# Optimization experiments

Hardware: AMD Instinct MI355X
Metric: run time of the kernel (lower is better)

## Reference

```python
import jax, jax.numpy as jnp
import numpy as np

DG = 4      # deformable groups
KS = 3      # kernel size
PAD = (KS - 1) // 2


def _deform_conv2d(x, offset, weight, dg=DG, pad=PAD):
    """Deformable conv v1 (stride 1, dilation 1, same padding, no bias).
    x:      [B, Cin, H, W]
    offset: [B, dg*2*K, H, W], layout (g, k, {y,x}) in channel dim
    weight: [Cout, Cin, kh, kw]
    """
    B, Cin, H, W = x.shape
    Cout, _, kh, kw = weight.shape
    K = kh * kw
    Cg = Cin // dg
    off = offset.reshape(B, dg, K, 2, H, W)
    # kernel tap coordinates, flattened row-major
    ky = jnp.repeat(jnp.arange(kh), kw).astype(x.dtype)   # [K]
    kx = jnp.tile(jnp.arange(kw), kh).astype(x.dtype)     # [K]
    # sampling positions [B, dg, K, H, W]
    py = off[:, :, :, 0] + (jnp.arange(H, dtype=x.dtype)[None, None, None, :, None]
                            + ky[None, None, :, None, None] - pad)
    px = off[:, :, :, 1] + (jnp.arange(W, dtype=x.dtype)[None, None, None, None, :]
                            + kx[None, None, :, None, None] - pad)
    y0 = jnp.floor(py)
    x0 = jnp.floor(px)
    xg = x.reshape(B, dg, Cg, H * W)
    val = jnp.zeros((B, dg, Cg, K, H, W), x.dtype)
    for dy in (0.0, 1.0):
        for dx in (0.0, 1.0):
            yc = y0 + dy
            xc = x0 + dx
            w = (1.0 - jnp.abs(py - yc)) * (1.0 - jnp.abs(px - xc))
            valid = (yc >= 0) & (yc <= H - 1) & (xc >= 0) & (xc <= W - 1)
            w = jnp.where(valid, w, 0.0)                      # zero padding
            idx = (jnp.clip(yc, 0, H - 1).astype(jnp.int32) * W
                   + jnp.clip(xc, 0, W - 1).astype(jnp.int32))  # [B,dg,K,H,W]
            idx_b = jnp.broadcast_to(idx.reshape(B, dg, 1, K * H * W),
                                     (B, dg, Cg, K * H * W))
            g = jnp.take_along_axis(xg, idx_b, axis=3).reshape(B, dg, Cg, K, H, W)
            val = val + w[:, :, None] * g
    # grouped-offset but dense conv: contract over (dg, Cg, K)
    wk = weight.reshape(Cout, dg, Cg, K)
    return jnp.einsum('bgckhw,ogck->bohw', val, wk)


def setup_inputs() -> dict:
    key = jax.random.key(0)
    k1, k2, k3, k4, k5, k6 = jax.random.split(key, 6)
    B, C, H, W = 2, 256, 64, 64
    reg_feat = jax.random.normal(k1, (B, C, H, W), jnp.float32)
    cls_feat = jax.random.normal(k2, (B, C, H, W), jnp.float32)
    pred_init = jax.random.normal(k3, (B, 34, H, W), jnp.float32)
    w_offset = jax.random.normal(k4, (DG * 2 * KS * KS, 34), jnp.float32) * 0.1
    w_reg = jax.random.normal(k5, (C, C, KS, KS), jnp.float32) * 0.01
    w_cls = jax.random.normal(k6, (C, C, KS, KS), jnp.float32) * 0.01
    return {"reg_feat": reg_feat, "cls_feat": cls_feat, "pred_init": pred_init,
            "w_offset": w_offset, "w_reg": w_reg, "w_cls": w_cls}


def reference(reg_feat, cls_feat, pred_init, w_offset, w_reg, w_cls):
    # 1x1 conv (bias-free) predicting offsets from detached anchor predictions
    offset = jnp.einsum('oc,bchw->bohw', w_offset, jax.lax.stop_gradient(pred_init))
    reg_refine = jax.nn.relu(_deform_conv2d(reg_feat, offset, w_reg))
    cls_refine = jax.nn.relu(_deform_conv2d(cls_feat, offset, w_cls))
    return (reg_refine, cls_refine)
```

## Files before the change

### kernel.cpp

```cpp
#include <hip/hip_runtime.h>
#include <hip/hip_bf16.h>
#include <stdint.h>

#define HW   4096
#define NB   2

typedef float f32x4 __attribute__((ext_vector_type(4)));
typedef short s16x8 __attribute__((ext_vector_type(8)));

__device__ __forceinline__ unsigned short f2bf(float f) {
    union { float f; unsigned int u; } v; v.f = f;
    unsigned int u = v.u;
    unsigned int r = (u + 0x7FFFu + ((u >> 16) & 1u)) >> 16;
    return (unsigned short)r;
}

__device__ __forceinline__ float bf2f(unsigned short u) {
    union { unsigned int u; float f; } v; v.u = ((unsigned int)u) << 16;
    return v.f;
}

__global__ void __launch_bounds__(256)
k_prep(const float* __restrict__ pred, const float* __restrict__ wo,
       const float* __restrict__ regf, const float* __restrict__ clsf,
       const float* __restrict__ wr,   const float* __restrict__ wc,
       float4* __restrict__ wbuf, int4* __restrict__ ibuf,
       unsigned short* __restrict__ fbuf, unsigned short* __restrict__ wfrag) {
    int bb = blockIdx.x;
    if (bb < 1152) {
        int loc = bb * 256 + threadIdx.x;
        int p  = loc & 4095;
        int g  = (loc >> 12) & 3;
        int bk = loc >> 14;
        int b  = bk / 9;
        int k  = bk - b * 9;
        int rowy = ((g * 9 + k) * 2) * 34;
        float oy = 0.f, ox = 0.f;
        const float* pb = pred + (size_t)b * 34 * HW + p;
        #pragma unroll
        for (int c = 0; c < 34; ++c) {
            float pv = pb[c * HW];
            oy += wo[rowy + c]      * pv;
            ox += wo[rowy + 34 + c] * pv;
        }
        int h = p >> 6, w = p & 63;
        int ky = k / 3, kx = k - ky * 3;
        float py = oy + (float)(h + ky - 1);
        float px = ox + (float)(w + kx - 1);
        float fy0 = floorf(py), fx0 = floorf(px);
        int y0 = (int)fy0, x0 = (int)fx0;
        float fy = py - fy0, fx = px - fx0;
        float wy0 = 1.f - fy, wy1 = fy, wx0 = 1.f - fx, wx1 = fx;
        if (!(y0 >= 0  && y0 <= 63)) wy0 = 0.f;
        if (!(y0 >= -1 && y0 <= 62)) wy1 = 0.f;
        if (!(x0 >= 0  && x0 <= 63)) wx0 = 0.f;
        if (!(x0 >= -1 && x0 <= 62)) wx1 = 0.f;
        int cy0 = min(max(y0, 0), 63),     cy1 = min(max(y0 + 1, 0), 63);
        int cx0 = min(max(x0, 0), 63),     cx1 = min(max(x0 + 1, 0), 63);
        wbuf[loc] = make_float4(wy0 * wx0, wy0 * wx1, wy1 * wx0, wy1 * wx1);
        ibuf[loc] = make_int4((cy0 * 64 + cx0) << 9, (cy0 * 64 + cx1) << 9,
                              (cy1 * 64 + cx0) << 9, (cy1 * 64 + cx1) << 9);
    } else if (bb < 2176) {
        __shared__ float tile[64][65];
        int bid = bb - 1152;
        int pt = bid & 63;
        int cb = (bid >> 6) & 3;
        int b  = (bid >> 8) & 1;
        int cv = bid >> 9;
        const float* src = cv ? clsf : regf;
        int t = threadIdx.x;
        int pl = t & 63, q = t >> 6;
        #pragma unroll
        for (int i = 0; i < 16; ++i) {
            int cl = q + i * 4;
            tile[cl][pl] = src[((size_t)(b * 256 + cb * 64 + cl)) * HW + pt * 64 + pl];
        }
        __syncthreads();
        int cpair = t & 31, prow = t >> 5;
        #pragma unroll
        for (int i = 0; i < 8; ++i) {
            int p = i * 8 + prow;
            unsigned int u0 = f2bf(tile[cpair * 2][p]);
            unsigned int u1 = f2bf(tile[cpair * 2 + 1][p]);
            *(unsigned int*)&fbuf[((size_t)((cv * 2 + b) * HW + pt * 64 + p)) * 256
                                  + cb * 64 + cpair * 2] = u0 | (u1 << 16);
        }
    } else {
        int L = (bb - 2176) * 256 + threadIdx.x;
        int conv = L / 73728;
        int r = L - conv * 73728;
        int lane = r & 63;
        int ot = (r >> 6) & 15;
        int kk = (r >> 10) & 1;
        int s  = r >> 11;
        int k = s >> 2, g = s & 3;
        int o  = ot * 16 + (lane & 15);
        int cb = kk * 32 + (lane >> 4) * 8;
        const float* w = conv ? wc : wr;
        s16x8 v;
        #pragma unroll
        for (int j = 0; j < 8; ++j) {
            int c = cb + j;
            v[j] = (short)f2bf(w[((size_t)o * 256 + g * 64 + c) * 9 + k]);
        }
        *(s16x8*)(wfrag + (size_t)L * 8) = v;
    }
}

__global__ void __launch_bounds__(512, 2)
k_main(const float4* __restrict__ wbuf, const int4* __restrict__ ibuf,
       const unsigned short* __restrict__ fbuf, const unsigned short* __restrict__ wfrag,
       float* __restrict__ out) {
    __shared__ __align__(16) unsigned short vt[2][64][72];

    int bid0 = blockIdx.x;
    int bid = (bid0 & 7) * 32 + (bid0 >> 3);
    int conv = bid >> 7;
    int b    = (bid >> 6) & 1;
    int pt   = bid & 63;
    int p0   = pt * 64;

    int tid  = threadIdx.x;
    int lane = tid & 63;
    int wo   = tid >> 6;
    int px   = tid >> 3;
    int cg   = tid & 7;

    const char* fbb = (const char*)(fbuf + (size_t)(conv * 2 + b) * HW * 256);
    const unsigned short* wfc = wfrag + (size_t)conv * 73728 * 8;

    f32x4 acc[2][4];
    #pragma unroll
    for (int i = 0; i < 2; ++i)
        #pragma unroll
        for (int j = 0; j < 4; ++j)
            acc[i][j] = (f32x4){0.f, 0.f, 0.f, 0.f};

    struct Par { float4 w4; int4 io; };
    struct Gat { s16x8 a, b, c, d; };

    auto ldpar = [&](int s) -> Par {
        int k = s >> 2, g = s & 3;
        int pidx = ((b * 9 + k) * 4 + g) * HW + p0 + px;
        Par P; P.w4 = wbuf[pidx]; P.io = ibuf[pidx];
        return P;
    };

    auto gather = [&](const Par& P, int g) -> Gat {
        const char* base = fbb + g * 128 + cg * 16;
        Gat G;
        G.a = *(const s16x8*)(base + P.io.x);
        G.b = *(const s16x8*)(base + P.io.y);
        G.c = *(const s16x8*)(base + P.io.z);
        G.d = *(const s16x8*)(base + P.io.w);
        return G;
    };

    auto finish = [&](const Par& P, const Gat& G, int buf) {
        float r[8];
        #pragma unroll
        for (int j = 0; j < 8; ++j) {
            r[j] = P.w4.x * bf2f((unsigned short)G.a[j])
                 + P.w4.y * bf2f((unsigned short)G.b[j])
                 + P.w4.z * bf2f((unsigned short)G.c[j])
                 + P.w4.w * bf2f((unsigned short)G.d[j]);
        }
        s16x8 pk;
        #pragma unroll
        for (int j = 0; j < 8; ++j) pk[j] = (short)f2bf(r[j]);
        *(s16x8*)&vt[buf][px][cg * 8] = pk;
    };

    s16x8 af00, af01, af10, af11;
    auto loadA = [&](int s) {
        const unsigned short* wfs = wfc + (size_t)s * 2048 * 8;
        af00 = *(const s16x8*)(wfs + ((size_t)( 0 + wo * 2 + 0) * 64 + lane) * 8);
        af01 = *(const s16x8*)(wfs + ((size_t)( 0 + wo * 2 + 1) * 64 + lane) * 8);
        af10 = *(const s16x8*)(wfs + ((size_t)(16 + wo * 2 + 0) * 64 + lane) * 8);
        af11 = *(const s16x8*)(wfs + ((size_t)(16 + wo * 2 + 1) * 64 + lane) * 8);
    };

    auto domfma = [&](int s) {
        s16x8 bfr[4];
        #pragma unroll
        for (int np = 0; np < 4; ++np)
            bfr[np] = *(const s16x8*)
                &vt[s & 1][np * 16 + (lane & 15)][(lane >> 4) * 8];
        #pragma unroll
        for (int np = 0; np < 4; ++np)
            acc[0][np] = __builtin_amdgcn_mfma_f32_16x16x32_bf16(af00, bfr[np],
                                                                 acc[0][np], 0, 0, 0);
        #pragma unroll
        for (int np = 0; np < 4; ++np)
            acc[1][np] = __builtin_amdgcn_mfma_f32_16x16x32_bf16(af01, bfr[np],
                                                                 acc[1][np], 0, 0, 0);
        #pragma unroll
        for (int np = 0; np < 4; ++np)
            bfr[np] = *(const s16x8*)
                &vt[s & 1][np * 16 + (lane & 15)][32 + (lane >> 4) * 8];
        #pragma unroll
        for (int np = 0; np < 4; ++np)
            acc[0][np] = __builtin_amdgcn_mfma_f32_16x16x32_bf16(af10, bfr[np],
                                                                 acc[0][np], 0, 0, 0);
        #pragma unroll
        for (int np = 0; np < 4; ++np)
            acc[1][np] = __builtin_amdgcn_mfma_f32_16x16x32_bf16(af11, bfr[np],
                                                                 acc[1][np], 0, 0, 0);
    };

    loadA(0);
    Par pc = ldpar(0);
    Par pn = ldpar(1);
    Gat gc = gather(pc, 0);
    finish(pc, gc, 0);

    for (int s = 0; s < 36; ++s) {
        Gat gn;
        Par p2 = pn;
        bool hasn = (s + 1 < 36);
        if (hasn)        gn = gather(pn, (s + 1) & 3);
        if (s + 2 < 36)  p2 = ldpar(s + 2);
        asm volatile("s_waitcnt lgkmcnt(0)" ::: "memory");
        __builtin_amdgcn_s_barrier();
        domfma(s);
        if (hasn) {
            loadA(s + 1);
            finish(pn, gn, (s + 1) & 1);
        }
        pn = p2;
    }

    float* ob = out + (size_t)conv * (NB * 256 * HW) + (size_t)b * 256 * HW;
    #pragma unroll
    for (int mo = 0; mo < 2; ++mo)
        #pragma unroll
        for (int np = 0; np < 4; ++np)
            #pragma unroll
            for (int r = 0; r < 4; ++r) {
                int o = wo * 32 + mo * 16 + (lane >> 4) * 4 + r;
                int p = p0 + np * 16 + (lane & 15);
                float v = acc[mo][np][r];
                ob[(size_t)o * HW + p] = v > 0.f ? v : 0.f;
            }
}

extern "C" void kernel_launch(void* const* d_in, const int* in_sizes, int n_in,
                              void* d_out, int out_size, void* d_ws, size_t ws_size,
                              hipStream_t stream) {
    (void)in_sizes; (void)n_in; (void)out_size; (void)ws_size;
    const float* reg_feat = (const float*)d_in[0];
    const float* cls_feat = (const float*)d_in[1];
    const float* pred     = (const float*)d_in[2];
    const float* w_off    = (const float*)d_in[3];
    const float* w_reg    = (const float*)d_in[4];
    const float* w_cls    = (const float*)d_in[5];
    float* out = (float*)d_out;
    char* ws = (char*)d_ws;
    float4*         wbuf  = (float4*)ws;
    int4*           ibuf  = (int4*)(ws + 4718592);
    unsigned short* fbuf  = (unsigned short*)(ws + 9437184);
    unsigned short* wfrag = (unsigned short*)(ws + 17825792);

    k_prep<<<2752, 256, 0, stream>>>(pred, w_off, reg_feat, cls_feat, w_reg, w_cls,
                                     wbuf, ibuf, fbuf, wfrag);
    k_main<<< 256, 512, 0, stream>>>(wbuf, ibuf, fbuf, wfrag, out);
}
```

Before: 52.46 us.

## Compute offsets and bilinear params inside main kernel, store packed fp16 params in LDS

The offset 1x1 conv and the bilinear weight/index computation move out of the prep kernel into a prologue of the main kernel. Each block now computes params for its own 64-pixel row and stores them in LDS as packed fp16 weights plus 16-bit indices. This removes the global wbuf/ibuf round trip and the 1152 prep blocks, and switches bf16 packing to a hardware v_cvt_pk_bf16_f32. The cost is redundant offset computation, since the reg and cls convs both recompute the same params, plus added LDS use and fp16 precision for the interpolation weights.

Result: slower. 64.09 us (+22.2%).

```diff
diff --git a/kernel.cpp b/kernel.cpp
--- a/kernel.cpp
+++ b/kernel.cpp
@@ -20,49 +20,22 @@
     return v.f;
 }
 
+__device__ __forceinline__ unsigned short f2h(float f) {
+    union { _Float16 h; unsigned short u; } v; v.h = (_Float16)f; return v.u;
+}
+
+__device__ __forceinline__ float h2f(unsigned short u) {
+    union { unsigned short u; _Float16 h; } v; v.u = u; return (float)v.h;
+}
+
 __global__ void __launch_bounds__(256)
-k_prep(const float* __restrict__ pred, const float* __restrict__ wo,
-       const float* __restrict__ regf, const float* __restrict__ clsf,
+k_prep(const float* __restrict__ regf, const float* __restrict__ clsf,
        const float* __restrict__ wr,   const float* __restrict__ wc,
-       float4* __restrict__ wbuf, int4* __restrict__ ibuf,
        unsigned short* __restrict__ fbuf, unsigned short* __restrict__ wfrag) {
     int bb = blockIdx.x;
-    if (bb < 1152) {
-        int loc = bb * 256 + threadIdx.x;
-        int p  = loc & 4095;
-        int g  = (loc >> 12) & 3;
-        int bk = loc >> 14;
-        int b  = bk / 9;
-        int k  = bk - b * 9;
-        int rowy = ((g * 9 + k) * 2) * 34;
-        float oy = 0.f, ox = 0.f;
-        const float* pb = pred + (size_t)b * 34 * HW + p;
-        #pragma unroll
-        for (int c = 0; c < 34; ++c) {
-            float pv = pb[c * HW];
-            oy += wo[rowy + c]      * pv;
-            ox += wo[rowy + 34 + c] * pv;
-        }
-        int h = p >> 6, w = p & 63;
-        int ky = k / 3, kx = k - ky * 3;
-        float py = oy + (float)(h + ky - 1);
-        float px = ox + (float)(w + kx - 1);
-        float fy0 = floorf(py), fx0 = floorf(px);
-        int y0 = (int)fy0, x0 = (int)fx0;
-        float fy = py - fy0, fx = px - fx0;
-        float wy0 = 1.f - fy, wy1 = fy, wx0 = 1.f - fx, wx1 = fx;
-        if (!(y0 >= 0  && y0 <= 63)) wy0 = 0.f;
-        if (!(y0 >= -1 && y0 <= 62)) wy1 = 0.f;
-        if (!(x0 >= 0  && x0 <= 63)) wx0 = 0.f;
-        if (!(x0 >= -1 && x0 <= 62)) wx1 = 0.f;
-        int cy0 = min(max(y0, 0), 63),     cy1 = min(max(y0 + 1, 0), 63);
-        int cx0 = min(max(x0, 0), 63),     cx1 = min(max(x0 + 1, 0), 63);
-        wbuf[loc] = make_float4(wy0 * wx0, wy0 * wx1, wy1 * wx0, wy1 * wx1);
-        ibuf[loc] = make_int4((cy0 * 64 + cx0) << 9, (cy0 * 64 + cx1) << 9,
-                              (cy1 * 64 + cx0) << 9, (cy1 * 64 + cx1) << 9);
-    } else if (bb < 2176) {
+    if (bb < 1024) {
         __shared__ float tile[64][65];
-        int bid = bb - 1152;
+        int bid = bb;
         int pt = bid & 63;
         int cb = (bid >> 6) & 3;
         int b  = (bid >> 8) & 1;
@@ -86,7 +59,7 @@
                                   + cb * 64 + cpair * 2] = u0 | (u1 << 16);
         }
     } else {
-        int L = (bb - 2176) * 256 + threadIdx.x;
+        int L = (bb - 1024) * 256 + threadIdx.x;
         int conv = L / 73728;
         int r = L - conv * 73728;
         int lane = r & 63;
@@ -108,10 +81,11 @@
 }
 
 __global__ void __launch_bounds__(512, 2)
-k_main(const float4* __restrict__ wbuf, const int4* __restrict__ ibuf,
+k_main(const float* __restrict__ pred, const float* __restrict__ woff,
        const unsigned short* __restrict__ fbuf, const unsigned short* __restrict__ wfrag,
        float* __restrict__ out) {
     __shared__ __align__(16) unsigned short vt[2][64][72];
+    __shared__ __align__(16) unsigned short par_lds[36][64][8];
 
     int bid0 = blockIdx.x;
     int bid = (bid0 & 7) * 32 + (bid0 >> 3);
@@ -122,12 +96,65 @@
 
     int tid  = threadIdx.x;
     int lane = tid & 63;
-    int wo   = tid >> 6;
+    int wv   = tid >> 6;
     int px   = tid >> 3;
     int cg   = tid & 7;
 
     const char* fbb = (const char*)(fbuf + (size_t)(conv * 2 + b) * HW * 256);
     const unsigned short* wfc = wfrag + (size_t)conv * 73728 * 8;
+
+    {
+        int j   = wv;
+        int lpx = lane;
+        const float* pb = pred + (size_t)b * 34 * HW + p0 + lpx;
+        float oyA[5], oxA[5];
+        #pragma unroll
+        for (int t = 0; t < 5; ++t) { oyA[t] = 0.f; oxA[t] = 0.f; }
+        for (int c = 0; c < 34; ++c) {
+            float pv = pb[c * HW];
+            #pragma unroll
+            for (int t = 0; t < 5; ++t) {
+                int s = j + t * 8;
+                if (s < 36) {
+                    int k = s >> 2, g = s & 3;
+                    int row = ((g * 9 + k) * 2) * 34;
+                    oyA[t] += woff[row + c]      * pv;
+                    oxA[t] += woff[row + 34 + c] * pv;
+                }
+            }
+        }
+        #pragma unroll
+        for (int t = 0; t < 5; ++t) {
+            int s = j + t * 8;
+            if (s < 36) {
+                int k = s >> 2;
+                int ky = k / 3, kx = k - ky * 3;
+                float py = oyA[t] + (float)(pt  + ky - 1);
+                float pxf = oxA[t] + (float)(lpx + kx - 1);
+                float fy0 = floorf(py), fx0 = floorf(pxf);
+                int y0 = (int)fy0, x0 = (int)fx0;
+                float fy = py - fy0, fx = pxf - fx0;
+                float wy0 = 1.f - fy, wy1 = fy, wx0 = 1.f - fx, wx1 = fx;
+                if (!(y0 >= 0  && y0 <= 63)) wy0 = 0.f;
+                if (!(y0 >= -1 && y0 <= 62)) wy1 = 0.f;
+                if (!(x0 >= 0  && x0 <= 63)) wx0 = 0.f;
+                if (!(x0 >= -1 && x0 <= 62)) wx1 = 0.f;
+                int cy0 = min(max(y0, 0), 63),     cy1 = min(max(y0 + 1, 0), 63);
+                int cx0 = min(max(x0, 0), 63),     cx1 = min(max(x0 + 1, 0), 63);
+                s16x8 pk;
+                pk[0] = (short)f2h(wy0 * wx0);
+                pk[1] = (short)f2h(wy0 * wx1);
+                pk[2] = (short)f2h(wy1 * wx0);
+                pk[3] = (short)f2h(wy1 * wx1);
+                pk[4] = (short)(unsigned short)(cy0 * 64 + cx0);
+                pk[5] = (short)(unsigned short)(cy0 * 64 + cx1);
+                pk[6] = (short)(unsigned short)(cy1 * 64 + cx0);
+                pk[7] = (short)(unsigned short)(cy1 * 64 + cx1);
+                *(s16x8*)&par_lds[s][lpx][0] = pk;
+            }
+        }
+    }
+    __syncthreads();
 
     f32x4 acc[2][4];
     #pragma unroll
@@ -136,23 +163,30 @@
         for (int j = 0; j < 4; ++j)
             acc[i][j] = (f32x4){0.f, 0.f, 0.f, 0.f};
 
-    struct Par { float4 w4; int4 io; };
+    struct Par { float w0, w1, w2, w3; int o0, o1, o2, o3; };
     struct Gat { s16x8 a, b, c, d; };
 
     auto ldpar = [&](int s) -> Par {
-        int k = s >> 2, g = s & 3;
-        int pidx = ((b * 9 + k) * 4 + g) * HW + p0 + px;
-        Par P; P.w4 = wbuf[pidx]; P.io = ibuf[pidx];
+        s16x8 raw = *(const s16x8*)&par_lds[s][px][0];
+        Par P;
+        P.w0 = h2f((unsigned short)raw[0]);
+        P.w1 = h2f((unsigned short)raw[1]);
+        P.w2 = h2f((unsigned short)raw[2]);
+        P.w3 = h2f((unsigned short)raw[3]);
+        P.o0 = ((int)(unsigned short)raw[4]) << 9;
+        P.o1 = ((int)(unsigned short)raw[5]) << 9;
+        P.o2 = ((int)(unsigned short)raw[6]) << 9;
+        P.o3 = ((int)(unsigned short)raw[7]) << 9;
         return P;
     };
 
     auto gather = [&](const Par& P, int g) -> Gat {
         const char* base = fbb + g * 128 + cg * 16;
         Gat G;
-        G.a = *(const s16x8*)(base + P.io.x);
-        G.b = *(const s16x8*)(base + P.io.y);
-        G.c = *(const s16x8*)(base + P.io.z);
-        G.d = *(const s16x8*)(base + P.io.w);
+        G.a = *(const s16x8*)(base + P.o0);
+        G.b = *(const s16x8*)(base + P.o1);
+        G.c = *(const s16x8*)(base + P.o2);
+        G.d = *(const s16x8*)(base + P.o3);
         return G;
     };
 
@@ -160,24 +194,28 @@
         float r[8];
         #pragma unroll
         for (int j = 0; j < 8; ++j) {
-            r[j] = P.w4.x * bf2f((unsigned short)G.a[j])
-                 + P.w4.y * bf2f((unsigned short)G.b[j])
-                 + P.w4.z * bf2f((unsigned short)G.c[j])
-                 + P.w4.w * bf2f((unsigned short)G.d[j]);
-        }
-        s16x8 pk;
-        #pragma unroll
-        for (int j = 0; j < 8; ++j) pk[j] = (short)f2bf(r[j]);
-        *(s16x8*)&vt[buf][px][cg * 8] = pk;
+            r[j] = P.w0 * bf2f((unsigned short)G.a[j])
+                 + P.w1 * bf2f((unsigned short)G.b[j])
+                 + P.w2 * bf2f((unsigned short)G.c[j])
+                 + P.w3 * bf2f((unsigned short)G.d[j]);
+        }
+        unsigned int q0, q1, q2, q3;
+        asm("v_cvt_pk_bf16_f32 %0, %1, %2" : "=v"(q0) : "v"(r[0]), "v"(r[1]));
+        asm("v_cvt_pk_bf16_f32 %0, %1, %2" : "=v"(q1) : "v"(r[2]), "v"(r[3]));
+        asm("v_cvt_pk_bf16_f32 %0, %1, %2" : "=v"(q2) : "v"(r[4]), "v"(r[5]));
+        asm("v_cvt_pk_bf16_f32 %0, %1, %2" : "=v"(q3) : "v"(r[6]), "v"(r[7]));
+        union { unsigned int q[4]; s16x8 v; } U;
+        U.q[0] = q0; U.q[1] = q1; U.q[2] = q2; U.q[3] = q3;
+        *(s16x8*)&vt[buf][px][cg * 8] = U.v;
     };
 
     s16x8 af00, af01, af10, af11;
     auto loadA = [&](int s) {
         const unsigned short* wfs = wfc + (size_t)s * 2048 * 8;
-        af00 = *(const s16x8*)(wfs + ((size_t)( 0 + wo * 2 + 0) * 64 + lane) * 8);
-        af01 = *(const s16x8*)(wfs + ((size_t)( 0 + wo * 2 + 1) * 64 + lane) * 8);
-        af10 = *(const s16x8*)(wfs + ((size_t)(16 + wo * 2 + 0) * 64 + lane) * 8);
-        af11 = *(const s16x8*)(wfs + ((size_t)(16 + wo * 2 + 1) * 64 + lane) * 8);
+        af00 = *(const s16x8*)(wfs + ((size_t)( 0 + wv * 2 + 0) * 64 + lane) * 8);
+        af01 = *(const s16x8*)(wfs + ((size_t)( 0 + wv * 2 + 1) * 64 + lane) * 8);
+        af10 = *(const s16x8*)(wfs + ((size_t)(16 + wv * 2 + 0) * 64 + lane) * 8);
+        af11 = *(const s16x8*)(wfs + ((size_t)(16 + wv * 2 + 1) * 64 + lane) * 8);
     };
 
     auto domfma = [&](int s) {
@@ -237,7 +275,7 @@
         for (int np = 0; np < 4; ++np)
             #pragma unroll
             for (int r = 0; r < 4; ++r) {
-                int o = wo * 32 + mo * 16 + (lane >> 4) * 4 + r;
+                int o = wv * 32 + mo * 16 + (lane >> 4) * 4 + r;
                 int p = p0 + np * 16 + (lane & 15);
                 float v = acc[mo][np][r];
                 ob[(size_t)o * HW + p] = v > 0.f ? v : 0.f;
@@ -256,12 +294,9 @@
     const float* w_cls    = (const float*)d_in[5];
     float* out = (float*)d_out;
     char* ws = (char*)d_ws;
-    float4*         wbuf  = (float4*)ws;
-    int4*           ibuf  = (int4*)(ws + 4718592);
-    unsigned short* fbuf  = (unsigned short*)(ws + 9437184);
-    unsigned short* wfrag = (unsigned short*)(ws + 17825792);
-
-    k_prep<<<2752, 256, 0, stream>>>(pred, w_off, reg_feat, cls_feat, w_reg, w_cls,
-                                     wbuf, ibuf, fbuf, wfrag);
-    k_main<<< 256, 512, 0, stream>>>(wbuf, ibuf, fbuf, wfrag, out);
-}
+    unsigned short* fbuf  = (unsigned short*)ws;
+    unsigned short* wfrag = (unsigned short*)(ws + 8388608);
+
+    k_prep<<<1600, 256, 0, stream>>>(reg_feat, cls_feat, w_reg, w_cls, fbuf, wfrag);
+    k_main<<< 256, 512, 0, stream>>>(pred, w_off, fbuf, wfrag, out);
+}
```

## Warp-specialize main kernel into gather producer waves and MFMA consumer waves

Applied to the files above, without the earlier changes.

Splits the 8 waves of each block into 4 producer waves that do bilinear gathers and write bf16 tiles into the double-buffered LDS, and 4 consumer waves that only run MFMAs and hold a larger 64x64 output tile each. Every producer thread now handles two pixels per step. The aim is to overlap the latency-bound gather work with matrix math instead of interleaving both in every wave. In exchange, each consumer wave keeps more accumulators and A fragments in registers, and the lockstep barrier count must match exactly between the two roles, so any imbalance between them stalls the pipeline.

New measurement: 54.87 us. 1.05x slower.

```diff
diff --git a/kernel.cpp b/kernel.cpp
--- a/kernel.cpp
+++ b/kernel.cpp
@@ -122,126 +122,134 @@
 
     int tid  = threadIdx.x;
     int lane = tid & 63;
-    int wo   = tid >> 6;
-    int px   = tid >> 3;
-    int cg   = tid & 7;
+    int wv   = tid >> 6;
 
     const char* fbb = (const char*)(fbuf + (size_t)(conv * 2 + b) * HW * 256);
     const unsigned short* wfc = wfrag + (size_t)conv * 73728 * 8;
 
-    f32x4 acc[2][4];
-    #pragma unroll
-    for (int i = 0; i < 2; ++i)
-        #pragma unroll
-        for (int j = 0; j < 4; ++j)
-            acc[i][j] = (f32x4){0.f, 0.f, 0.f, 0.f};
-
-    struct Par { float4 w4; int4 io; };
-    struct Gat { s16x8 a, b, c, d; };
-
-    auto ldpar = [&](int s) -> Par {
-        int k = s >> 2, g = s & 3;
-        int pidx = ((b * 9 + k) * 4 + g) * HW + p0 + px;
-        Par P; P.w4 = wbuf[pidx]; P.io = ibuf[pidx];
-        return P;
-    };
-
-    auto gather = [&](const Par& P, int g) -> Gat {
-        const char* base = fbb + g * 128 + cg * 16;
-        Gat G;
-        G.a = *(const s16x8*)(base + P.io.x);
-        G.b = *(const s16x8*)(base + P.io.y);
-        G.c = *(const s16x8*)(base + P.io.z);
-        G.d = *(const s16x8*)(base + P.io.w);
-        return G;
-    };
-
-    auto finish = [&](const Par& P, const Gat& G, int buf) {
-        float r[8];
-        #pragma unroll
-        for (int j = 0; j < 8; ++j) {
-            r[j] = P.w4.x * bf2f((unsigned short)G.a[j])
-                 + P.w4.y * bf2f((unsigned short)G.b[j])
-                 + P.w4.z * bf2f((unsigned short)G.c[j])
-                 + P.w4.w * bf2f((unsigned short)G.d[j]);
-        }
-        s16x8 pk;
-        #pragma unroll
-        for (int j = 0; j < 8; ++j) pk[j] = (short)f2bf(r[j]);
-        *(s16x8*)&vt[buf][px][cg * 8] = pk;
-    };
-
-    s16x8 af00, af01, af10, af11;
-    auto loadA = [&](int s) {
-        const unsigned short* wfs = wfc + (size_t)s * 2048 * 8;
-        af00 = *(const s16x8*)(wfs + ((size_t)( 0 + wo * 2 + 0) * 64 + lane) * 8);
-        af01 = *(const s16x8*)(wfs + ((size_t)( 0 + wo * 2 + 1) * 64 + lane) * 8);
-        af10 = *(const s16x8*)(wfs + ((size_t)(16 + wo * 2 + 0) * 64 + lane) * 8);
-        af11 = *(const s16x8*)(wfs + ((size_t)(16 + wo * 2 + 1) * 64 + lane) * 8);
-    };
-
-    auto domfma = [&](int s) {
-        s16x8 bfr[4];
-        #pragma unroll
-        for (int np = 0; np < 4; ++np)
-            bfr[np] = *(const s16x8*)
-                &vt[s & 1][np * 16 + (lane & 15)][(lane >> 4) * 8];
-        #pragma unroll
-        for (int np = 0; np < 4; ++np)
-            acc[0][np] = __builtin_amdgcn_mfma_f32_16x16x32_bf16(af00, bfr[np],
-                                                                 acc[0][np], 0, 0, 0);
-        #pragma unroll
-        for (int np = 0; np < 4; ++np)
-            acc[1][np] = __builtin_amdgcn_mfma_f32_16x16x32_bf16(af01, bfr[np],
-                                                                 acc[1][np], 0, 0, 0);
-        #pragma unroll
-        for (int np = 0; np < 4; ++np)
-            bfr[np] = *(const s16x8*)
-                &vt[s & 1][np * 16 + (lane & 15)][32 + (lane >> 4) * 8];
-        #pragma unroll
-        for (int np = 0; np < 4; ++np)
-            acc[0][np] = __builtin_amdgcn_mfma_f32_16x16x32_bf16(af10, bfr[np],
-                                                                 acc[0][np], 0, 0, 0);
-        #pragma unroll
-        for (int np = 0; np < 4; ++np)
-            acc[1][np] = __builtin_amdgcn_mfma_f32_16x16x32_bf16(af11, bfr[np],
-                                                                 acc[1][np], 0, 0, 0);
-    };
-
-    loadA(0);
-    Par pc = ldpar(0);
-    Par pn = ldpar(1);
-    Gat gc = gather(pc, 0);
-    finish(pc, gc, 0);
-
-    for (int s = 0; s < 36; ++s) {
-        Gat gn;
-        Par p2 = pn;
-        bool hasn = (s + 1 < 36);
-        if (hasn)        gn = gather(pn, (s + 1) & 3);
-        if (s + 2 < 36)  p2 = ldpar(s + 2);
+    if (wv < 4) {
+        int px0 = tid >> 3;
+        int cg  = tid & 7;
+
+        struct Par { float w0, w1, w2, w3; int o0, o1, o2, o3; };
+        struct Gat { s16x8 a, b, c, d; };
+
+        auto ldpar = [&](int s, int dpx) -> Par {
+            int k = s >> 2, g = s & 3;
+            int pidx = ((b * 9 + k) * 4 + g) * HW + p0 + px0 + dpx;
+            float4 w4 = wbuf[pidx];
+            int4   io = ibuf[pidx];
+            Par P;
+            P.w0 = w4.x; P.w1 = w4.y; P.w2 = w4.z; P.w3 = w4.w;
+            P.o0 = io.x; P.o1 = io.y; P.o2 = io.z; P.o3 = io.w;
+            return P;
+        };
+
+        auto gather = [&](const Par& P, int g) -> Gat {
+            const char* base = fbb + g * 128 + cg * 16;
+            Gat G;
+            G.a = *(const s16x8*)(base + P.o0);
+            G.b = *(const s16x8*)(base + P.o1);
+            G.c = *(const s16x8*)(base + P.o2);
+            G.d = *(const s16x8*)(base + P.o3);
+            return G;
+        };
+
+        auto finish = [&](const Par& P, const Gat& G, int px, int buf) {
+            float r[8];
+            #pragma unroll
+            for (int j = 0; j < 8; ++j) {
+                r[j] = P.w0 * bf2f((unsigned short)G.a[j])
+                     + P.w1 * bf2f((unsigned short)G.b[j])
+                     + P.w2 * bf2f((unsigned short)G.c[j])
+                     + P.w3 * bf2f((unsigned short)G.d[j]);
+            }
+            s16x8 pk;
+            #pragma unroll
+            for (int j = 0; j < 8; ++j) pk[j] = (short)f2bf(r[j]);
+            *(s16x8*)&vt[buf][px][cg * 8] = pk;
+        };
+
+        Par pa = ldpar(0, 0),  pb = ldpar(0, 32);
+        Par na = ldpar(1, 0),  nb = ldpar(1, 32);
+        Gat ga = gather(pa, 0), gb = gather(pb, 0);
+        finish(pa, ga, px0, 0);
+        finish(pb, gb, px0 + 32, 0);
+        Par fa = ldpar(2, 0),  fbp = ldpar(2, 32);
+        ga = gather(na, 1); gb = gather(nb, 1);
         asm volatile("s_waitcnt lgkmcnt(0)" ::: "memory");
         __builtin_amdgcn_s_barrier();
-        domfma(s);
-        if (hasn) {
-            loadA(s + 1);
-            finish(pn, gn, (s + 1) & 1);
-        }
-        pn = p2;
+
+        for (int i = 1; i < 36; ++i) {
+            Gat g2a, g2b;
+            if (i < 35) { g2a = gather(fa, (i + 1) & 3); g2b = gather(fbp, (i + 1) & 3); }
+            Par p3a = fa, p3b = fbp;
+            if (i < 34) { p3a = ldpar(i + 2, 0); p3b = ldpar(i + 2, 32); }
+            finish(na, ga, px0, i & 1);
+            finish(nb, gb, px0 + 32, i & 1);
+            na = fa; nb = fbp; fa = p3a; fbp = p3b;
+            ga = g2a; gb = g2b;
+            asm volatile("s_waitcnt lgkmcnt(0)" ::: "memory");
+            __builtin_amdgcn_s_barrier();
+        }
+    } else {
+        int cw = wv - 4;
+
+        f32x4 acc[4][4];
+        #pragma unroll
+        for (int i = 0; i < 4; ++i)
+            #pragma unroll
+            for (int j = 0; j < 4; ++j)
+                acc[i][j] = (f32x4){0.f, 0.f, 0.f, 0.f};
+
+        s16x8 af[2][4];
+        auto loadA = [&](int s) {
+            const unsigned short* wfs = wfc + (size_t)s * 2048 * 8;
+            #pragma unroll
+            for (int kk = 0; kk < 2; ++kk)
+                #pragma unroll
+                for (int mo = 0; mo < 4; ++mo)
+                    af[kk][mo] = *(const s16x8*)
+                        (wfs + ((size_t)(kk * 16 + cw * 4 + mo) * 64 + lane) * 8);
+        };
+
+        loadA(0);
+        __builtin_amdgcn_s_barrier();
+
+        for (int s = 0; s < 36; ++s) {
+            #pragma unroll
+            for (int kk = 0; kk < 2; ++kk) {
+                s16x8 bfr[4];
+                #pragma unroll
+                for (int np = 0; np < 4; ++np)
+                    bfr[np] = *(const s16x8*)
+                        &vt[s & 1][np * 16 + (lane & 15)][kk * 32 + (lane >> 4) * 8];
+                #pragma unroll
+                for (int mo = 0; mo < 4; ++mo)
+                    #pragma unroll
+                    for (int np = 0; np < 4; ++np)
+                        acc[mo][np] = __builtin_amdgcn_mfma_f32_16x16x32_bf16(
+                            af[kk][mo], bfr[np], acc[mo][np], 0, 0, 0);
+            }
+            if (s < 35) {
+                loadA(s + 1);
+                __builtin_amdgcn_s_barrier();
+            }
+        }
+
+        float* ob = out + (size_t)conv * (NB * 256 * HW) + (size_t)b * 256 * HW;
+        #pragma unroll
+        for (int mo = 0; mo < 4; ++mo)
+            #pragma unroll
+            for (int np = 0; np < 4; ++np)
+                #pragma unroll
+                for (int r = 0; r < 4; ++r) {
+                    int o = cw * 64 + mo * 16 + (lane >> 4) * 4 + r;
+                    int p = p0 + np * 16 + (lane & 15);
+                    float v = acc[mo][np][r];
+                    ob[(size_t)o * HW + p] = v > 0.f ? v : 0.f;
+                }
     }
-
-    float* ob = out + (size_t)conv * (NB * 256 * HW) + (size_t)b * 256 * HW;
-    #pragma unroll
-    for (int mo = 0; mo < 2; ++mo)
-        #pragma unroll
-        for (int np = 0; np < 4; ++np)
-            #pragma unroll
-            for (int r = 0; r < 4; ++r) {
-                int o = wo * 32 + mo * 16 + (lane >> 4) * 4 + r;
-                int p = p0 + np * 16 + (lane & 15);
-                float v = acc[mo][np][r];
-                ob[(size_t)o * HW + p] = v > 0.f ? v : 0.f;
-            }
 }
 
 extern "C" void kernel_launch(void* const* d_in, const int* in_sizes, int n_in,
```

## Deepen gather pipeline and compute all offset taps per pixel in prep

Applied to the files above, without the earlier changes.

In the prep kernel, each thread now loads the 34 pred channels for one pixel once into registers and computes all 36 (k,g) offset/bilinear entries, instead of one entry per thread re-reading pred. Offset blocks move to the end of the grid, which shrinks from 2752 to 1632 blocks. The main kernel's software pipeline now issues the gather two stages ahead instead of one, to hide more global gather latency. The cost is more live registers (an extra Gat of four s16x8 plus an extra Par), which may pressure the 2-wave-per-SIMD launch bound. The offset blocks also get fewer threads, with 32 serial dot products each.

Result: slower. 79.22 us (+51.0%).

```diff
diff --git a/kernel.cpp b/kernel.cpp
--- a/kernel.cpp
+++ b/kernel.cpp
@@ -27,42 +27,9 @@
        float4* __restrict__ wbuf, int4* __restrict__ ibuf,
        unsigned short* __restrict__ fbuf, unsigned short* __restrict__ wfrag) {
     int bb = blockIdx.x;
-    if (bb < 1152) {
-        int loc = bb * 256 + threadIdx.x;
-        int p  = loc & 4095;
-        int g  = (loc >> 12) & 3;
-        int bk = loc >> 14;
-        int b  = bk / 9;
-        int k  = bk - b * 9;
-        int rowy = ((g * 9 + k) * 2) * 34;
-        float oy = 0.f, ox = 0.f;
-        const float* pb = pred + (size_t)b * 34 * HW + p;
-        #pragma unroll
-        for (int c = 0; c < 34; ++c) {
-            float pv = pb[c * HW];
-            oy += wo[rowy + c]      * pv;
-            ox += wo[rowy + 34 + c] * pv;
-        }
-        int h = p >> 6, w = p & 63;
-        int ky = k / 3, kx = k - ky * 3;
-        float py = oy + (float)(h + ky - 1);
-        float px = ox + (float)(w + kx - 1);
-        float fy0 = floorf(py), fx0 = floorf(px);
-        int y0 = (int)fy0, x0 = (int)fx0;
-        float fy = py - fy0, fx = px - fx0;
-        float wy0 = 1.f - fy, wy1 = fy, wx0 = 1.f - fx, wx1 = fx;
-        if (!(y0 >= 0  && y0 <= 63)) wy0 = 0.f;
-        if (!(y0 >= -1 && y0 <= 62)) wy1 = 0.f;
-        if (!(x0 >= 0  && x0 <= 63)) wx0 = 0.f;
-        if (!(x0 >= -1 && x0 <= 62)) wx1 = 0.f;
-        int cy0 = min(max(y0, 0), 63),     cy1 = min(max(y0 + 1, 0), 63);
-        int cx0 = min(max(x0, 0), 63),     cx1 = min(max(x0 + 1, 0), 63);
-        wbuf[loc] = make_float4(wy0 * wx0, wy0 * wx1, wy1 * wx0, wy1 * wx1);
-        ibuf[loc] = make_int4((cy0 * 64 + cx0) << 9, (cy0 * 64 + cx1) << 9,
-                              (cy1 * 64 + cx0) << 9, (cy1 * 64 + cx1) << 9);
-    } else if (bb < 2176) {
+    if (bb < 1024) {
         __shared__ float tile[64][65];
-        int bid = bb - 1152;
+        int bid = bb;
         int pt = bid & 63;
         int cb = (bid >> 6) & 3;
         int b  = (bid >> 8) & 1;
@@ -85,8 +52,8 @@
             *(unsigned int*)&fbuf[((size_t)((cv * 2 + b) * HW + pt * 64 + p)) * 256
                                   + cb * 64 + cpair * 2] = u0 | (u1 << 16);
         }
-    } else {
-        int L = (bb - 2176) * 256 + threadIdx.x;
+    } else if (bb < 1600) {
+        int L = (bb - 1024) * 256 + threadIdx.x;
         int conv = L / 73728;
         int r = L - conv * 73728;
         int lane = r & 63;
@@ -104,6 +71,45 @@
             v[j] = (short)f2bf(w[((size_t)o * 256 + g * 64 + c) * 9 + k]);
         }
         *(s16x8*)(wfrag + (size_t)L * 8) = v;
+    } else {
+        int q = bb - 1600;
+        int b = q >> 4;
+        int p = (q & 15) * 256 + threadIdx.x;
+        float pv[34];
+        const float* pb = pred + (size_t)b * 34 * HW + p;
+        #pragma unroll
+        for (int c = 0; c < 34; ++c) pv[c] = pb[c * HW];
+        int h = p >> 6, w = p & 63;
+        #pragma unroll
+        for (int k = 0; k < 9; ++k) {
+            int ky = k / 3, kx = k - ky * 3;
+            #pragma unroll
+            for (int g = 0; g < 4; ++g) {
+                int rowy = ((g * 9 + k) * 2) * 34;
+                float oy = 0.f, ox = 0.f;
+                #pragma unroll
+                for (int c = 0; c < 34; ++c) {
+                    oy += wo[rowy + c]      * pv[c];
+                    ox += wo[rowy + 34 + c] * pv[c];
+                }
+                float py = oy + (float)(h + ky - 1);
+                float px = ox + (float)(w + kx - 1);
+                float fy0 = floorf(py), fx0 = floorf(px);
+                int y0 = (int)fy0, x0 = (int)fx0;
+                float fy = py - fy0, fx = px - fx0;
+                float wy0 = 1.f - fy, wy1 = fy, wx0 = 1.f - fx, wx1 = fx;
+                if (!(y0 >= 0  && y0 <= 63)) wy0 = 0.f;
+                if (!(y0 >= -1 && y0 <= 62)) wy1 = 0.f;
+                if (!(x0 >= 0  && x0 <= 63)) wx0 = 0.f;
+                if (!(x0 >= -1 && x0 <= 62)) wx1 = 0.f;
+                int cy0 = min(max(y0, 0), 63),     cy1 = min(max(y0 + 1, 0), 63);
+                int cx0 = min(max(x0, 0), 63),     cx1 = min(max(x0 + 1, 0), 63);
+                int loc = ((b * 9 + k) * 4 + g) * HW + p;
+                wbuf[loc] = make_float4(wy0 * wx0, wy0 * wx1, wy1 * wx0, wy1 * wx1);
+                ibuf[loc] = make_int4((cy0 * 64 + cx0) << 9, (cy0 * 64 + cx1) << 9,
+                                      (cy1 * 64 + cx0) << 9, (cy1 * 64 + cx1) << 9);
+            }
+        }
     }
 }
 
@@ -122,7 +128,7 @@
 
     int tid  = threadIdx.x;
     int lane = tid & 63;
-    int wo   = tid >> 6;
+    int wv   = tid >> 6;
     int px   = tid >> 3;
     int cg   = tid & 7;
 
@@ -174,10 +180,10 @@
     s16x8 af00, af01, af10, af11;
     auto loadA = [&](int s) {
         const unsigned short* wfs = wfc + (size_t)s * 2048 * 8;
-        af00 = *(const s16x8*)(wfs + ((size_t)( 0 + wo * 2 + 0) * 64 + lane) * 8);
-        af01 = *(const s16x8*)(wfs + ((size_t)( 0 + wo * 2 + 1) * 64 + lane) * 8);
-        af10 = *(const s16x8*)(wfs + ((size_t)(16 + wo * 2 + 0) * 64 + lane) * 8);
-        af11 = *(const s16x8*)(wfs + ((size_t)(16 + wo * 2 + 1) * 64 + lane) * 8);
+        af00 = *(const s16x8*)(wfs + ((size_t)( 0 + wv * 2 + 0) * 64 + lane) * 8);
+        af01 = *(const s16x8*)(wfs + ((size_t)( 0 + wv * 2 + 1) * 64 + lane) * 8);
+        af10 = *(const s16x8*)(wfs + ((size_t)(16 + wv * 2 + 0) * 64 + lane) * 8);
+        af11 = *(const s16x8*)(wfs + ((size_t)(16 + wv * 2 + 1) * 64 + lane) * 8);
     };
 
     auto domfma = [&](int s) {
@@ -209,25 +215,26 @@
     };
 
     loadA(0);
-    Par pc = ldpar(0);
-    Par pn = ldpar(1);
-    Gat gc = gather(pc, 0);
-    finish(pc, gc, 0);
+    Par P0 = ldpar(0);
+    Gat G0 = gather(P0, 0);
+    finish(P0, G0, 0);
+    Par P1 = ldpar(1);
+    Par P2 = ldpar(2);
+    Gat G1 = gather(P1, 1);
 
     for (int s = 0; s < 36; ++s) {
-        Gat gn;
-        Par p2 = pn;
-        bool hasn = (s + 1 < 36);
-        if (hasn)        gn = gather(pn, (s + 1) & 3);
-        if (s + 2 < 36)  p2 = ldpar(s + 2);
+        Gat Gn;
+        Par Pn;
+        if (s + 2 < 36) Gn = gather(P2, (s + 2) & 3);
+        Pn = (s + 3 < 36) ? ldpar(s + 3) : P2;
         asm volatile("s_waitcnt lgkmcnt(0)" ::: "memory");
         __builtin_amdgcn_s_barrier();
         domfma(s);
-        if (hasn) {
+        if (s + 1 < 36) {
             loadA(s + 1);
-            finish(pn, gn, (s + 1) & 1);
-        }
-        pn = p2;
+            finish(P1, G1, (s + 1) & 1);
+        }
+        P1 = P2; P2 = Pn; G1 = Gn;
     }
 
     float* ob = out + (size_t)conv * (NB * 256 * HW) + (size_t)b * 256 * HW;
@@ -237,7 +244,7 @@
         for (int np = 0; np < 4; ++np)
             #pragma unroll
             for (int r = 0; r < 4; ++r) {
-                int o = wo * 32 + mo * 16 + (lane >> 4) * 4 + r;
+                int o = wv * 32 + mo * 16 + (lane >> 4) * 4 + r;
                 int p = p0 + np * 16 + (lane & 15);
                 float v = acc[mo][np][r];
                 ob[(size_t)o * HW + p] = v > 0.f ? v : 0.f;
@@ -261,7 +268,7 @@
     unsigned short* fbuf  = (unsigned short*)(ws + 9437184);
     unsigned short* wfrag = (unsigned short*)(ws + 17825792);
 
-    k_prep<<<2752, 256, 0, stream>>>(pred, w_off, reg_feat, cls_feat, w_reg, w_cls,
+    k_prep<<<1632, 256, 0, stream>>>(pred, w_off, reg_feat, cls_feat, w_reg, w_cls,
                                      wbuf, ibuf, fbuf, wfrag);
     k_main<<< 256, 512, 0, stream>>>(wbuf, ibuf, fbuf, wfrag, out);
 }
```
